# Kernel tuning notes

Hardware: AMD Instinct MI355X
Metric: run time of the kernel (lower is better)

Reference implementation:

```python
import jax, jax.numpy as jnp
import numpy as np

B, N, E, NREG, DIN, F = 16, 20000, 640000, 2000, 128, 32
NEG_SLOPE = 0.2  # PyG GATConv default negative_slope


def setup_inputs() -> dict:
    key = jax.random.key(0)
    ks = jax.random.split(key, 10)
    x = jax.random.normal(ks[0], (B, N, DIN), dtype=jnp.float32)
    edge_src = jnp.sort(jax.random.randint(ks[1], (E,), 0, NREG, dtype=jnp.int64))
    edge_dst = jax.random.randint(ks[2], (E,), 0, N, dtype=jnp.int64)
    edge_attr = jax.random.uniform(ks[3], (B, E, 1), dtype=jnp.float32)
    # GATConv parameters (heads=1, concat=False, edge_dim=1)
    W = jax.random.normal(ks[4], (DIN, F), dtype=jnp.float32) * 0.05   # lin (shared src/dst)
    att_src = jax.random.normal(ks[5], (F,), dtype=jnp.float32) * 0.1
    att_dst = jax.random.normal(ks[6], (F,), dtype=jnp.float32) * 0.1
    lin_edge = jax.random.normal(ks[7], (1, F), dtype=jnp.float32) * 0.1
    att_edge = jax.random.normal(ks[8], (F,), dtype=jnp.float32) * 0.1
    bias = jax.random.normal(ks[9], (F,), dtype=jnp.float32) * 0.01
    return {"x": x, "edge_attr": edge_attr, "W": W, "att_src": att_src,
            "att_dst": att_dst, "lin_edge": lin_edge, "att_edge": att_edge,
            "bias": bias, "edge_src": edge_src, "edge_dst": edge_dst}


def _gat_regulon(x, eattr, W, att_src, att_dst, lin_edge, att_edge, bias,
                 src, dst):
    # x: [N, DIN], eattr: [E, 1]; src/dst: [E] int (src < NREG, sorted)
    h = x @ W                                  # [N, F]
    a_src = h @ att_src                        # [N]
    a_dst = h @ att_dst                        # [N]
    # add_self_loops=True with fill_value='mean' for edge_attr
    loop_attr = jnp.broadcast_to(jnp.mean(eattr, axis=0, keepdims=True), (N, 1))
    eattr_full = jnp.concatenate([eattr, loop_attr], axis=0)         # [E+N, 1]
    sl = jnp.arange(N, dtype=src.dtype)
    src_f = jnp.concatenate([src, sl])                               # [E+N]
    dst_f = jnp.concatenate([dst, sl])                               # [E+N]
    a_edge = (eattr_full @ lin_edge) @ att_edge                      # [E+N]
    alpha = jax.nn.leaky_relu(a_src[src_f] + a_dst[dst_f] + a_edge, NEG_SLOPE)
    # segment softmax over destination nodes (self-loops => no empty segment)
    m = jax.ops.segment_max(alpha, dst_f, num_segments=N)
    ex = jnp.exp(alpha - m[dst_f])
    s = jax.ops.segment_sum(ex, dst_f, num_segments=N)
    coef = ex / s[dst_f]                                             # [E+N]
    rep = jax.ops.segment_sum(coef[:, None] * h[src_f], dst_f, num_segments=N)
    rep = rep + bias                                                 # [N, F]
    # fused regulon pooling: out[i] = rep[i] + sum_{(i->t) in E} rep[t]
    pooled = jax.ops.segment_sum(rep[dst], src, num_segments=NREG)   # [NREG, F]
    return rep[:NREG] + pooled


def reference(x, edge_attr, W, att_src, att_dst, lin_edge, att_edge, bias,
              edge_src, edge_dst):
    fn = jax.vmap(lambda xi, ei: _gat_regulon(xi, ei, W, att_src, att_dst,
                                              lin_edge, att_edge, bias,
                                              edge_src, edge_dst))
    return fn(x, edge_attr)                                          # [B, NREG, F]
```

## Files before the change

kernel.cpp:

```cpp
#include <hip/hip_runtime.h>
#include <math.h>

#define B    16
#define N    20000
#define E    640000
#define NREG 2000
#define DIN  128
#define F    32
#define NEG  0.2f
#define BF   (B * F)
#define NCHUNK 8
#define CS   2500
#define HIST_BLOCKS 1024
#define SCAT_BLOCKS 1024

typedef unsigned int uint;

__device__ inline uint bf16pair(float a, float b) {
    uint ua = __float_as_uint(a); ua = (ua + 0x7fffu + ((ua >> 16) & 1u)) >> 16;
    uint ub = __float_as_uint(b); ub = (ub + 0x7fffu + ((ub >> 16) & 1u)) >> 16;
    return ua | (ub << 16);
}
__device__ inline float bf16lo(uint v) { return __uint_as_float(v << 16); }
__device__ inline float bf16hi(uint v) { return __uint_as_float(v & 0xffff0000u); }

__global__ __launch_bounds__(256) void k_prep1(const int* __restrict__ esrc,
                                               const int* __restrict__ edst,
                                               const float* __restrict__ eattr,
                                               const float* __restrict__ lin_edge,
                                               const float* __restrict__ att_edge,
                                               int* __restrict__ counts,
                                               int* __restrict__ roff,
                                               float* __restrict__ meanb,
                                               float* __restrict__ cedge) {
    int blk = blockIdx.x;
    int t = threadIdx.x;
    if (blk < HIST_BLOCKS) {
        {
            int b = blk >> 6, sl = blk & 63;
            const float4* base = (const float4*)(eattr + (size_t)b * E + sl * 10000);
            float s = 0.f;
            for (int i = t; i < 2500; i += 256) {
                float4 v = base[i];
                s += (v.x + v.y) + (v.z + v.w);
            }
            __shared__ float sh[256];
            sh[t] = s;
            __syncthreads();
            for (int d = 128; d > 0; d >>= 1) {
                if (t < d) sh[t] += sh[t + d];
                __syncthreads();
            }
            if (t == 0) atomicAdd(&meanb[b], sh[0]);
        }
        for (int e = blk * 256 + t; e < E; e += HIST_BLOCKS * 256)
            atomicAdd(&counts[edst[e]], 1);
    } else if (blk < HIST_BLOCKS + 8) {
        int r = (blk - HIST_BLOCKS) * 256 + t;
        if (r > NREG) return;
        int lo = 0, hi = E;
        while (lo < hi) {
            int mid = (lo + hi) >> 1;
            if (esrc[mid] < r) lo = mid + 1; else hi = mid;
        }
        roff[r] = lo;
    } else {
        if (t == 0) {
            float s = 0.f;
            for (int f = 0; f < F; ++f) s += lin_edge[f] * att_edge[f];
            *cedge = s;
        }
    }
}

__global__ __launch_bounds__(1024) void k_scan(const int* __restrict__ in,
                                               int* __restrict__ out, int n) {
    __shared__ int sh[1024];
    int t = threadIdx.x;
    int chunk = (n + 1023) / 1024;
    int lo = t * chunk;
    int hi = lo + chunk; if (hi > n) hi = n;
    int local = 0;
    for (int i = lo; i < hi; ++i) local += in[i];
    sh[t] = local;
    __syncthreads();
    for (int d = 1; d < 1024; d <<= 1) {
        int v = (t >= d) ? sh[t - d] : 0;
        __syncthreads();
        sh[t] += v;
        __syncthreads();
    }
    int run = (t == 0) ? 0 : sh[t - 1];
    for (int i = lo; i < hi; ++i) { out[i] = run; run += in[i]; }
    if (t == 1023) out[n] = sh[1023];
}

__global__ __launch_bounds__(256) void k_prep2(const int* __restrict__ esrc,
                                               const int* __restrict__ edst,
                                               const int* __restrict__ off,
                                               int* __restrict__ cursor,
                                               int* __restrict__ csr_src,
                                               int* __restrict__ csr_eid,
                                               const int* __restrict__ roff,
                                               int* __restrict__ boff,
                                               int* __restrict__ pe_dst) {
    __shared__ int cnt[NCHUNK], pref[NCHUNK], cur[NCHUNK];
    int blk = blockIdx.x;
    int t = threadIdx.x;
    if (blk < SCAT_BLOCKS) {
        int e = blk * 256 + t;
        for (; e < E; e += SCAT_BLOCKS * 256) {
            int d = edst[e];
            int pos = off[d] + atomicAdd(&cursor[d], 1);
            csr_src[pos] = esrc[e];
            csr_eid[pos] = e;
        }
    } else {
        int r = blk - SCAT_BLOCKS;
        int lo = roff[r], hi = roff[r + 1];
        if (t < NCHUNK) { cnt[t] = 0; cur[t] = 0; }
        __syncthreads();
        for (int e = lo + t; e < hi; e += 256)
            atomicAdd(&cnt[edst[e] / CS], 1);
        __syncthreads();
        if (t == 0) {
            int run = 0;
            #pragma unroll
            for (int c = 0; c < NCHUNK; ++c) { pref[c] = run; run += cnt[c]; }
        }
        __syncthreads();
        if (t < NCHUNK) boff[r * NCHUNK + t] = lo + pref[t];
        if (r == 0 && t == 0) boff[NREG * NCHUNK] = E;
        for (int e = lo + t; e < hi; e += 256) {
            int d = edst[e];
            int c = d / CS;
            int pos = lo + pref[c] + atomicAdd(&cur[c], 1);
            pe_dst[pos] = d;
        }
    }
}

__global__ __launch_bounds__(256) void k_trans(const float* __restrict__ eattr,
                                               const float* __restrict__ cedge,
                                               float* __restrict__ ew) {
    __shared__ float tile[256][17];
    int e0 = blockIdx.x * 256;
    int t = threadIdx.x;
    #pragma unroll
    for (int b = 0; b < B; ++b)
        tile[t][b] = eattr[(size_t)b * E + e0 + t];
    __syncthreads();
    float c = *cedge;
    #pragma unroll
    for (int p = 0; p < 4; ++p) {
        int i4 = (p * 256 + t) * 4;
        int el = i4 >> 4, b0 = i4 & 15;
        float4 o;
        o.x = c * tile[el][b0 + 0];
        o.y = c * tile[el][b0 + 1];
        o.z = c * tile[el][b0 + 2];
        o.w = c * tile[el][b0 + 3];
        *(float4*)&ew[(size_t)e0 * 16 + i4] = o;
    }
}

#define XS_LD 260
__global__ __launch_bounds__(256) void k_gemm(const float* __restrict__ x,
                                              const float* __restrict__ W,
                                              const float* __restrict__ att_src,
                                              const float* __restrict__ att_dst,
                                              uint* __restrict__ hu,
                                              float* __restrict__ a_src,
                                              float* __restrict__ a_dst) {
    __shared__ float Ws[DIN * F];
    __shared__ float xs[32 * XS_LD];
    int t = threadIdx.x;
    int row0 = blockIdx.x * 256;
    #pragma unroll
    for (int j = 0; j < 4; ++j) {
        int idx = (t + 256 * j) * 4;
        *(float4*)&Ws[idx] = *(const float4*)&W[idx];
    }
    const int lr = t & 63;
    const int fg = t >> 6;
    float acc[4][8];
    #pragma unroll
    for (int i = 0; i < 4; ++i)
        #pragma unroll
        for (int j = 0; j < 8; ++j) acc[i][j] = 0.f;

    for (int kc = 0; kc < 4; ++kc) {
        __syncthreads();
        #pragma unroll
        for (int j = 0; j < 8; ++j) {
            int p = t + 256 * j;
            int row = p >> 3;
            int kk  = (p & 7) * 4;
            float4 g = *(const float4*)&x[(size_t)(row0 + row) * DIN + kc * 32 + kk];
            xs[(kk + 0) * XS_LD + row] = g.x;
            xs[(kk + 1) * XS_LD + row] = g.y;
            xs[(kk + 2) * XS_LD + row] = g.z;
            xs[(kk + 3) * XS_LD + row] = g.w;
        }
        __syncthreads();
        #pragma unroll
        for (int k = 0; k < 32; ++k) {
            float4 xv = *(float4*)&xs[k * XS_LD + 4 * lr];
            float4 w0 = *(float4*)&Ws[(kc * 32 + k) * F + fg * 8];
            float4 w1 = *(float4*)&Ws[(kc * 32 + k) * F + fg * 8 + 4];
            float xr[4] = {xv.x, xv.y, xv.z, xv.w};
            float wr[8] = {w0.x, w0.y, w0.z, w0.w, w1.x, w1.y, w1.z, w1.w};
            #pragma unroll
            for (int i = 0; i < 4; ++i)
                #pragma unroll
                for (int j = 0; j < 8; ++j)
                    acc[i][j] = fmaf(xr[i], wr[j], acc[i][j]);
        }
    }
    #pragma unroll
    for (int i = 0; i < 4; ++i) {
        int row = row0 + lr * 4 + i;
        int b = row / N;
        int n = row - b * N;
        uint4 o;
        o.x = bf16pair(acc[i][0], acc[i][1]);
        o.y = bf16pair(acc[i][2], acc[i][3]);
        o.z = bf16pair(acc[i][4], acc[i][5]);
        o.w = bf16pair(acc[i][6], acc[i][7]);
        *(uint4*)&hu[(size_t)n * 256 + b * 16 + fg * 4] = o;
    }
    float* red = xs;
    __syncthreads();
    #pragma unroll
    for (int i = 0; i < 4; ++i) {
        float s1 = 0.f, s2 = 0.f;
        #pragma unroll
        for (int j = 0; j < 8; ++j) {
            float as = att_src[fg * 8 + j];
            float ad = att_dst[fg * 8 + j];
            s1 = fmaf(acc[i][j], as, s1);
            s2 = fmaf(acc[i][j], ad, s2);
        }
        red[fg * 256 + lr * 4 + i]        = s1;
        red[1024 + fg * 256 + lr * 4 + i] = s2;
    }
    __syncthreads();
    {
        float s1 = red[t] + red[256 + t] + red[512 + t] + red[768 + t];
        float s2 = red[1024 + t] + red[1280 + t] + red[1536 + t] + red[1792 + t];
        int row = row0 + t;
        int b = row / N;
        int n = row - b * N;
        a_src[(size_t)n * B + b] = s1;
        a_dst[(size_t)n * B + b] = s2;
    }
}

__global__ __launch_bounds__(256) void k_rep(
    const uint* __restrict__ hu, const float* __restrict__ a_src,
    const float* __restrict__ a_dst, const float* __restrict__ ew,
    const int* __restrict__ csr_eid,
    const float* __restrict__ bias, const float* __restrict__ meanb,
    const float* __restrict__ cedge, const int* __restrict__ dst_off,
    const int* __restrict__ csr_src, uint* __restrict__ repu) {
    int i = blockIdx.x;
    int t = threadIdx.x;
    int b  = t >> 4;
    int fp = t & 15;
    float c = *cedge;
    float adst = a_dst[(size_t)i * B + b];
    float meanv = meanb[b] * (1.f / (float)E);
    float al = a_src[(size_t)i * B + b] + adst + meanv * c;
    al = al > 0.f ? al : NEG * al;
    float wself = __expf(al);
    uint hv = hu[(size_t)i * 256 + t];
    float acc0 = wself * bf16lo(hv);
    float acc1 = wself * bf16hi(hv);
    float ssum = 0.f;
    int lo = dst_off[i], hi = dst_off[i + 1];
    for (int j = lo; j < hi; j += 16) {
        int jj = j + fp;
        int idx = jj < hi ? jj : hi - 1;
        int   sv_l = csr_src[idx];
        int   ev_l = csr_eid[idx];
        float a2 = a_src[(size_t)sv_l * B + b] + adst
                 + ew[(size_t)ev_l * B + b];
        a2 = a2 > 0.f ? a2 : NEG * a2;
        float w_l = (jj < hi) ? __expf(a2) : 0.f;
        ssum += w_l;
        #pragma unroll
        for (int q = 0; q < 16; ++q) {
            float wq = __shfl(w_l, q, 16);
            int   sq = __shfl(sv_l, q, 16);
            uint v = hu[(size_t)sq * 256 + t];
            acc0 = fmaf(wq, bf16lo(v), acc0);
            acc1 = fmaf(wq, bf16hi(v), acc1);
        }
    }
    #pragma unroll
    for (int d = 1; d < 16; d <<= 1) ssum += __shfl_xor(ssum, d, 16);
    float inv = 1.f / (wself + ssum);
    repu[(size_t)i * 256 + t] = bf16pair(acc0 * inv + bias[2 * fp],
                                         acc1 * inv + bias[2 * fp + 1]);
}

__global__ __launch_bounds__(256) void k_pool(const uint* __restrict__ repu,
                                              const int* __restrict__ boff,
                                              const int* __restrict__ pe_dst,
                                              float* __restrict__ partial) {
    int key = blockIdx.x;
    int c = key / NREG;
    int r = key - c * NREG;
    int idx = r * NCHUNK + c;
    int t = threadIdx.x;
    int lo = boff[idx], hi = boff[idx + 1];
    float acc0 = 0.f, acc1 = 0.f;
    int e = lo;
    for (; e + 8 <= hi; e += 8) {
        int d0 = pe_dst[e+0], d1 = pe_dst[e+1], d2 = pe_dst[e+2], d3 = pe_dst[e+3];
        int d4 = pe_dst[e+4], d5 = pe_dst[e+5], d6 = pe_dst[e+6], d7 = pe_dst[e+7];
        uint v0 = repu[(size_t)d0 * 256 + t];
        uint v1 = repu[(size_t)d1 * 256 + t];
        uint v2 = repu[(size_t)d2 * 256 + t];
        uint v3 = repu[(size_t)d3 * 256 + t];
        uint v4 = repu[(size_t)d4 * 256 + t];
        uint v5 = repu[(size_t)d5 * 256 + t];
        uint v6 = repu[(size_t)d6 * 256 + t];
        uint v7 = repu[(size_t)d7 * 256 + t];
        acc0 += (bf16lo(v0) + bf16lo(v1)) + (bf16lo(v2) + bf16lo(v3))
              + (bf16lo(v4) + bf16lo(v5)) + (bf16lo(v6) + bf16lo(v7));
        acc1 += (bf16hi(v0) + bf16hi(v1)) + (bf16hi(v2) + bf16hi(v3))
              + (bf16hi(v4) + bf16hi(v5)) + (bf16hi(v6) + bf16hi(v7));
    }
    for (; e < hi; ++e) {
        int d = pe_dst[e];
        uint v = repu[(size_t)d * 256 + t];
        acc0 += bf16lo(v);
        acc1 += bf16hi(v);
    }
    float2 o = {acc0, acc1};
    *(float2*)&partial[((size_t)r * NCHUNK + c) * BF + 2 * t] = o;
}

__global__ __launch_bounds__(256) void k_combine(const uint* __restrict__ repu,
                                                 const float* __restrict__ partial,
                                                 float* __restrict__ out) {
    int r = blockIdx.x;
    int t = threadIdx.x;
    int b  = t >> 4;
    int fp = t & 15;
    uint v = repu[(size_t)r * 256 + t];
    float s0 = bf16lo(v), s1 = bf16hi(v);
    #pragma unroll
    for (int c = 0; c < NCHUNK; ++c) {
        float2 p = *(const float2*)&partial[((size_t)r * NCHUNK + c) * BF + 2 * t];
        s0 += p.x; s1 += p.y;
    }
    float2 o = {s0, s1};
    *(float2*)&out[(size_t)b * NREG * F + r * F + 2 * fp] = o;
}

extern "C" void kernel_launch(void* const* d_in, const int* in_sizes, int n_in,
                              void* d_out, int out_size, void* d_ws, size_t ws_size,
                              hipStream_t stream) {
    const float* x        = (const float*)d_in[0];
    const float* eattr    = (const float*)d_in[1];
    const float* W        = (const float*)d_in[2];
    const float* att_src  = (const float*)d_in[3];
    const float* att_dst  = (const float*)d_in[4];
    const float* lin_edge = (const float*)d_in[5];
    const float* att_edge = (const float*)d_in[6];
    const float* bias     = (const float*)d_in[7];
    const int*   esrc     = (const int*)d_in[8];
    const int*   edst     = (const int*)d_in[9];
    float* out = (float*)d_out;

    char* ws = (char*)d_ws;
    size_t off = 0;
    auto alloc = [&](size_t bytes) -> void* {
        void* p = ws + off;
        off = (off + bytes + 255) & ~(size_t)255;
        return p;
    };
    uint*  hu    = (uint*)alloc((size_t)N * 256 * 4);
    uint*  repu  = (uint*)alloc((size_t)N * 256 * 4);
    float* ew    = (float*)alloc((size_t)E * B * 4);
    float* a_src = (float*)alloc((size_t)N * B * 4);
    float* a_dst = (float*)alloc((size_t)N * B * 4);
    int* dst_off = (int*)alloc((size_t)(N + 1) * 4);
    int* roff    = (int*)alloc((size_t)(NREG + 1) * 4);
    int* csr_src = (int*)alloc((size_t)E * 4);
    int* csr_eid = (int*)alloc((size_t)E * 4);
    int* pe_dst  = (int*)alloc((size_t)E * 4);
    int* boff    = (int*)alloc((size_t)(NREG * NCHUNK + 1) * 4);
    char* zbase   = ws + off;
    int* counts   = (int*)alloc((size_t)N * 4);
    int* cursor   = (int*)alloc((size_t)N * 4);
    float* meanb  = (float*)alloc((size_t)B * 4);
    float* cedge  = (float*)alloc(4);
    size_t zbytes = (size_t)((ws + off) - zbase);
    float* partial = ew;

    hipMemsetAsync(zbase, 0, zbytes, stream);

    k_prep1<<<HIST_BLOCKS + 8 + 1, 256, 0, stream>>>(esrc, edst, eattr, lin_edge,
                                                     att_edge, counts, roff,
                                                     meanb, cedge);
    k_scan<<<1, 1024, 0, stream>>>(counts, dst_off, N);
    k_prep2<<<SCAT_BLOCKS + NREG, 256, 0, stream>>>(esrc, edst, dst_off, cursor,
                                                    csr_src, csr_eid,
                                                    roff, boff, pe_dst);
    k_trans<<<E / 256, 256, 0, stream>>>(eattr, cedge, ew);
    k_gemm<<<(B * N) / 256, 256, 0, stream>>>(x, W, att_src, att_dst,
                                              hu, a_src, a_dst);
    k_rep<<<N, 256, 0, stream>>>(hu, a_src, a_dst, ew, csr_eid, bias, meanb,
                                 cedge, dst_off, csr_src, repu);
    k_pool<<<NREG * NCHUNK, 256, 0, stream>>>(repu, boff, pe_dst, partial);
    k_combine<<<NREG, 256, 0, stream>>>(repu, partial, out);
}
```

Measured before the change: 547.0 us.

## Pack CSR src/eid into int2 and widen k_rep gathers to uint2 with edge split

Merges the separate csr_src and csr_eid arrays into one int2 array so each edge needs one load. k_rep is reorganised so each thread gathers 8 bytes (4 bf16 features) per source row and handles half the edges, exchanging weights through double-buffered shared memory instead of shuffles. The two edge halves are combined with a cross-half shuffle. This aims to halve gather instruction count and improve memory coalescing in the dominant aggregation kernel, at the cost of a __syncthreads per 16-edge tile. k_trans is also moved after k_gemm in the launch order.

```diff
diff --git a/kernel.cpp b/kernel.cpp
--- a/kernel.cpp
+++ b/kernel.cpp
@@ -99,8 +99,7 @@
                                                const int* __restrict__ edst,
                                                const int* __restrict__ off,
                                                int* __restrict__ cursor,
-                                               int* __restrict__ csr_src,
-                                               int* __restrict__ csr_eid,
+                                               int2* __restrict__ csr_se,
                                                const int* __restrict__ roff,
                                                int* __restrict__ boff,
                                                int* __restrict__ pe_dst) {
@@ -112,8 +111,7 @@
         for (; e < E; e += SCAT_BLOCKS * 256) {
             int d = edst[e];
             int pos = off[d] + atomicAdd(&cursor[d], 1);
-            csr_src[pos] = esrc[e];
-            csr_eid[pos] = e;
+            csr_se[pos] = make_int2(esrc[e], e);
         }
     } else {
         int r = blk - SCAT_BLOCKS;
@@ -259,49 +257,78 @@
 __global__ __launch_bounds__(256) void k_rep(
     const uint* __restrict__ hu, const float* __restrict__ a_src,
     const float* __restrict__ a_dst, const float* __restrict__ ew,
-    const int* __restrict__ csr_eid,
+    const int2* __restrict__ csr_se,
     const float* __restrict__ bias, const float* __restrict__ meanb,
     const float* __restrict__ cedge, const int* __restrict__ dst_off,
-    const int* __restrict__ csr_src, uint* __restrict__ repu) {
+    uint* __restrict__ repu) {
+    __shared__ uint2 wsh[2][4][64];
     int i = blockIdx.x;
     int t = threadIdx.x;
-    int b  = t >> 4;
-    int fp = t & 15;
+    int w = t >> 6;
+    int l = t & 63;
+    int fpA = l & 15;
+    int bA  = (w << 2) + (l >> 4);
+    int epar = l >> 5;
+    int b4   = (l >> 3) & 3;
+    int bB   = (w << 2) + b4;
+    int u    = l & 7;
+    int laneoff = bB * 8 + u;
+
     float c = *cedge;
-    float adst = a_dst[(size_t)i * B + b];
-    float meanv = meanb[b] * (1.f / (float)E);
-    float al = a_src[(size_t)i * B + b] + adst + meanv * c;
+    int lo = dst_off[i], hi = dst_off[i + 1];
+    float adstA = a_dst[i * B + bA];
+    float ssum = 0.f;
+    float acc0 = 0.f, acc1 = 0.f, acc2 = 0.f, acc3 = 0.f;
+    const uint2* hu2 = (const uint2*)hu;
+
+    int nt = 0;
+    for (int j = lo; j < hi; j += 16, ++nt) {
+        int p = nt & 1;
+        int jj = j + fpA;
+        int idx = jj < hi ? jj : hi - 1;
+        int2 se = csr_se[idx];
+        float a2 = a_src[se.x * B + bA] + adstA + ew[se.y * B + bA];
+        a2 = a2 > 0.f ? a2 : NEG * a2;
+        float wv = (jj < hi) ? __expf(a2) : 0.f;
+        ssum += wv;
+        wsh[p][w][fpA * 4 + (l >> 4)] = make_uint2(__float_as_uint(wv), (uint)se.x);
+        __syncthreads();
+        #pragma unroll
+        for (int k = 0; k < 8; ++k) {
+            uint2 ws = wsh[p][w][(2 * k + epar) * 4 + b4];
+            float wq = __uint_as_float(ws.x);
+            uint2 v = hu2[(int)ws.y * 128 + laneoff];
+            acc0 = fmaf(wq, bf16lo(v.x), acc0);
+            acc1 = fmaf(wq, bf16hi(v.x), acc1);
+            acc2 = fmaf(wq, bf16lo(v.y), acc2);
+            acc3 = fmaf(wq, bf16hi(v.y), acc3);
+        }
+    }
+    #pragma unroll
+    for (int d = 1; d < 16; d <<= 1) ssum += __shfl_xor(ssum, d, 16);
+    float Sb = __shfl(ssum, b4 << 4, 64);
+    float meanv = meanb[bB] * (1.f / (float)E);
+    float al = a_src[i * B + bB] + a_dst[i * B + bB] + meanv * c;
     al = al > 0.f ? al : NEG * al;
     float wself = __expf(al);
-    uint hv = hu[(size_t)i * 256 + t];
-    float acc0 = wself * bf16lo(hv);
-    float acc1 = wself * bf16hi(hv);
-    float ssum = 0.f;
-    int lo = dst_off[i], hi = dst_off[i + 1];
-    for (int j = lo; j < hi; j += 16) {
-        int jj = j + fp;
-        int idx = jj < hi ? jj : hi - 1;
-        int   sv_l = csr_src[idx];
-        int   ev_l = csr_eid[idx];
-        float a2 = a_src[(size_t)sv_l * B + b] + adst
-                 + ew[(size_t)ev_l * B + b];
-        a2 = a2 > 0.f ? a2 : NEG * a2;
-        float w_l = (jj < hi) ? __expf(a2) : 0.f;
-        ssum += w_l;
-        #pragma unroll
-        for (int q = 0; q < 16; ++q) {
-            float wq = __shfl(w_l, q, 16);
-            int   sq = __shfl(sv_l, q, 16);
-            uint v = hu[(size_t)sq * 256 + t];
-            acc0 = fmaf(wq, bf16lo(v), acc0);
-            acc1 = fmaf(wq, bf16hi(v), acc1);
-        }
-    }
-    #pragma unroll
-    for (int d = 1; d < 16; d <<= 1) ssum += __shfl_xor(ssum, d, 16);
-    float inv = 1.f / (wself + ssum);
-    repu[(size_t)i * 256 + t] = bf16pair(acc0 * inv + bias[2 * fp],
-                                         acc1 * inv + bias[2 * fp + 1]);
+    if (epar == 0) {
+        uint2 hv = hu2[i * 128 + laneoff];
+        acc0 = fmaf(wself, bf16lo(hv.x), acc0);
+        acc1 = fmaf(wself, bf16hi(hv.x), acc1);
+        acc2 = fmaf(wself, bf16lo(hv.y), acc2);
+        acc3 = fmaf(wself, bf16hi(hv.y), acc3);
+    }
+    acc0 += __shfl_xor(acc0, 32, 64);
+    acc1 += __shfl_xor(acc1, 32, 64);
+    acc2 += __shfl_xor(acc2, 32, 64);
+    acc3 += __shfl_xor(acc3, 32, 64);
+    if (epar == 0) {
+        float inv = 1.f / (wself + Sb);
+        uint2 o;
+        o.x = bf16pair(acc0 * inv + bias[4 * u + 0], acc1 * inv + bias[4 * u + 1]);
+        o.y = bf16pair(acc2 * inv + bias[4 * u + 2], acc3 * inv + bias[4 * u + 3]);
+        ((uint2*)repu)[i * 128 + laneoff] = o;
+    }
 }
 
 __global__ __launch_bounds__(256) void k_pool(const uint* __restrict__ repu,
@@ -389,8 +416,7 @@
     float* a_dst = (float*)alloc((size_t)N * B * 4);
     int* dst_off = (int*)alloc((size_t)(N + 1) * 4);
     int* roff    = (int*)alloc((size_t)(NREG + 1) * 4);
-    int* csr_src = (int*)alloc((size_t)E * 4);
-    int* csr_eid = (int*)alloc((size_t)E * 4);
+    int2* csr_se = (int2*)alloc((size_t)E * 8);
     int* pe_dst  = (int*)alloc((size_t)E * 4);
     int* boff    = (int*)alloc((size_t)(NREG * NCHUNK + 1) * 4);
     char* zbase   = ws + off;
@@ -408,13 +434,12 @@
                                                      meanb, cedge);
     k_scan<<<1, 1024, 0, stream>>>(counts, dst_off, N);
     k_prep2<<<SCAT_BLOCKS + NREG, 256, 0, stream>>>(esrc, edst, dst_off, cursor,
-                                                    csr_src, csr_eid,
-                                                    roff, boff, pe_dst);
-    k_trans<<<E / 256, 256, 0, stream>>>(eattr, cedge, ew);
+                                                    csr_se, roff, boff, pe_dst);
     k_gemm<<<(B * N) / 256, 256, 0, stream>>>(x, W, att_src, att_dst,
                                               hu, a_src, a_dst);
-    k_rep<<<N, 256, 0, stream>>>(hu, a_src, a_dst, ew, csr_eid, bias, meanb,
-                                 cedge, dst_off, csr_src, repu);
+    k_trans<<<E / 256, 256, 0, stream>>>(eattr, cedge, ew);
+    k_rep<<<N, 256, 0, stream>>>(hu, a_src, a_dst, ew, csr_se, bias, meanb,
+                                 cedge, dst_off, repu);
     k_pool<<<NREG * NCHUNK, 256, 0, stream>>>(repu, boff, pe_dst, partial);
     k_combine<<<NREG, 256, 0, stream>>>(repu, partial, out);
 }
```

After: 546.6 us. Within noise of the previous version (-0.1%).

## Use fp16 storage and packed half2 FMA in attention aggregation kernel

Applied to the files above, without the earlier changes.

Switches h, rep and the per-edge attention term storage from bf16/fp32 to fp16, and restructures k_rep so each thread handles 8 features with packed half2 FMAs. Each wavefront processes 4 edges at a time, using DPP and readlane broadcasts, and the four wavefronts' partials are reduced through shared memory. CSR src and edge id are packed into int2, and partial gets its own buffer. This cuts memory traffic for the gathers and edge weights, and the FMA instruction count, at the cost of fp16 range and accumulation precision for weighted sums.

```diff
diff --git a/kernel.cpp b/kernel.cpp
--- a/kernel.cpp
+++ b/kernel.cpp
@@ -1,4 +1,5 @@
 #include <hip/hip_runtime.h>
+#include <hip/hip_fp16.h>
 #include <math.h>
 
 #define B    16
@@ -16,13 +17,13 @@
 
 typedef unsigned int uint;
 
-__device__ inline uint bf16pair(float a, float b) {
-    uint ua = __float_as_uint(a); ua = (ua + 0x7fffu + ((ua >> 16) & 1u)) >> 16;
-    uint ub = __float_as_uint(b); ub = (ub + 0x7fffu + ((ub >> 16) & 1u)) >> 16;
-    return ua | (ub << 16);
-}
-__device__ inline float bf16lo(uint v) { return __uint_as_float(v << 16); }
-__device__ inline float bf16hi(uint v) { return __uint_as_float(v & 0xffff0000u); }
+__device__ inline uint f16pair(float a, float b) {
+    __half2 h = __floats2half2_rn(a, b);
+    return *(uint*)&h;
+}
+__device__ inline float2 h2f2(uint v) {
+    return __half22float2(*(__half2*)&v);
+}
 
 __global__ __launch_bounds__(256) void k_prep1(const int* __restrict__ esrc,
                                                const int* __restrict__ edst,
@@ -99,8 +100,7 @@
                                                const int* __restrict__ edst,
                                                const int* __restrict__ off,
                                                int* __restrict__ cursor,
-                                               int* __restrict__ csr_src,
-                                               int* __restrict__ csr_eid,
+                                               int2* __restrict__ csr_se,
                                                const int* __restrict__ roff,
                                                int* __restrict__ boff,
                                                int* __restrict__ pe_dst) {
@@ -112,8 +112,7 @@
         for (; e < E; e += SCAT_BLOCKS * 256) {
             int d = edst[e];
             int pos = off[d] + atomicAdd(&cursor[d], 1);
-            csr_src[pos] = esrc[e];
-            csr_eid[pos] = e;
+            csr_se[pos] = make_int2(esrc[e], e);
         }
     } else {
         int r = blk - SCAT_BLOCKS;
@@ -142,7 +141,7 @@
 
 __global__ __launch_bounds__(256) void k_trans(const float* __restrict__ eattr,
                                                const float* __restrict__ cedge,
-                                               float* __restrict__ ew) {
+                                               __half* __restrict__ ew) {
     __shared__ float tile[256][17];
     int e0 = blockIdx.x * 256;
     int t = threadIdx.x;
@@ -155,12 +154,10 @@
     for (int p = 0; p < 4; ++p) {
         int i4 = (p * 256 + t) * 4;
         int el = i4 >> 4, b0 = i4 & 15;
-        float4 o;
-        o.x = c * tile[el][b0 + 0];
-        o.y = c * tile[el][b0 + 1];
-        o.z = c * tile[el][b0 + 2];
-        o.w = c * tile[el][b0 + 3];
-        *(float4*)&ew[(size_t)e0 * 16 + i4] = o;
+        uint2 o;
+        o.x = f16pair(c * tile[el][b0 + 0], c * tile[el][b0 + 1]);
+        o.y = f16pair(c * tile[el][b0 + 2], c * tile[el][b0 + 3]);
+        *(uint2*)&ew[(size_t)e0 * 16 + i4] = o;
     }
 }
 
@@ -223,10 +220,10 @@
         int b = row / N;
         int n = row - b * N;
         uint4 o;
-        o.x = bf16pair(acc[i][0], acc[i][1]);
-        o.y = bf16pair(acc[i][2], acc[i][3]);
-        o.z = bf16pair(acc[i][4], acc[i][5]);
-        o.w = bf16pair(acc[i][6], acc[i][7]);
+        o.x = f16pair(acc[i][0], acc[i][1]);
+        o.y = f16pair(acc[i][2], acc[i][3]);
+        o.z = f16pair(acc[i][4], acc[i][5]);
+        o.w = f16pair(acc[i][6], acc[i][7]);
         *(uint4*)&hu[(size_t)n * 256 + b * 16 + fg * 4] = o;
     }
     float* red = xs;
@@ -257,51 +254,98 @@
 }
 
 __global__ __launch_bounds__(256) void k_rep(
-    const uint* __restrict__ hu, const float* __restrict__ a_src,
-    const float* __restrict__ a_dst, const float* __restrict__ ew,
-    const int* __restrict__ csr_eid,
-    const float* __restrict__ bias, const float* __restrict__ meanb,
-    const float* __restrict__ cedge, const int* __restrict__ dst_off,
-    const int* __restrict__ csr_src, uint* __restrict__ repu) {
+    const uint4* __restrict__ hu4, const float* __restrict__ a_src,
+    const float* __restrict__ a_dst, const __half* __restrict__ ew,
+    const int2* __restrict__ csr_se, const float* __restrict__ bias,
+    const float* __restrict__ meanb, const float* __restrict__ cedge,
+    const int* __restrict__ dst_off, uint4* __restrict__ repu4) {
+    __shared__ uint4 lacc[4][64];
+    __shared__ float lsum[4][64];
     int i = blockIdx.x;
     int t = threadIdx.x;
-    int b  = t >> 4;
-    int fp = t & 15;
-    float c = *cedge;
+    int wid = t >> 6;
+    int l = t & 63;
+    int b = l >> 2;
+    int q = l & 3;
     float adst = a_dst[(size_t)i * B + b];
-    float meanv = meanb[b] * (1.f / (float)E);
-    float al = a_src[(size_t)i * B + b] + adst + meanv * c;
-    al = al > 0.f ? al : NEG * al;
-    float wself = __expf(al);
-    uint hv = hu[(size_t)i * 256 + t];
-    float acc0 = wself * bf16lo(hv);
-    float acc1 = wself * bf16hi(hv);
+    int lo = dst_off[i], hi = dst_off[i + 1];
     float ssum = 0.f;
-    int lo = dst_off[i], hi = dst_off[i + 1];
-    for (int j = lo; j < hi; j += 16) {
-        int jj = j + fp;
+    __half2 zero2 = __half2half2(__float2half(0.f));
+    __half2 acc0 = zero2, acc1 = zero2, acc2 = zero2, acc3 = zero2;
+
+    for (int g0 = lo + wid * 4; g0 < hi; g0 += 16) {
+        int jj = g0 + q;
         int idx = jj < hi ? jj : hi - 1;
-        int   sv_l = csr_src[idx];
-        int   ev_l = csr_eid[idx];
-        float a2 = a_src[(size_t)sv_l * B + b] + adst
-                 + ew[(size_t)ev_l * B + b];
+        int2 se = csr_se[idx];
+        float a2 = a_src[(size_t)se.x * B + b] + adst
+                 + __half2float(ew[(size_t)se.y * B + b]);
         a2 = a2 > 0.f ? a2 : NEG * a2;
-        float w_l = (jj < hi) ? __expf(a2) : 0.f;
-        ssum += w_l;
+        float wv = (jj < hi) ? __expf(a2) : 0.f;
+        ssum += wv;
+        __half2 w2 = __half2half2(__float2half(wv));
+        uint w2u = *(uint*)&w2;
+#define REP_STEP(EIDX, CTRL) { \
+        int wei = __builtin_amdgcn_mov_dpp((int)w2u, CTRL, 0xf, 0xf, true); \
+        __half2 weh = *(__half2*)&wei; \
+        int sre = __builtin_amdgcn_readlane(se.x, EIDX); \
+        uint4 hv = hu4[(size_t)sre * 64 + l]; \
+        acc0 = __hfma2(weh, *(__half2*)&hv.x, acc0); \
+        acc1 = __hfma2(weh, *(__half2*)&hv.y, acc1); \
+        acc2 = __hfma2(weh, *(__half2*)&hv.z, acc2); \
+        acc3 = __hfma2(weh, *(__half2*)&hv.w, acc3); }
+        REP_STEP(0, 0)
+        REP_STEP(1, 85)
+        REP_STEP(2, 170)
+        REP_STEP(3, 255)
+#undef REP_STEP
+    }
+    ssum += __shfl_xor(ssum, 1, 64);
+    ssum += __shfl_xor(ssum, 2, 64);
+    if (wid) {
+        uint4 a;
+        a.x = *(uint*)&acc0; a.y = *(uint*)&acc1;
+        a.z = *(uint*)&acc2; a.w = *(uint*)&acc3;
+        lacc[wid][l] = a;
+        lsum[wid][l] = ssum;
+    }
+    __syncthreads();
+    if (wid == 0) {
+        float2 p0 = __half22float2(acc0);
+        float2 p1 = __half22float2(acc1);
+        float2 p2 = __half22float2(acc2);
+        float2 p3 = __half22float2(acc3);
         #pragma unroll
-        for (int q = 0; q < 16; ++q) {
-            float wq = __shfl(w_l, q, 16);
-            int   sq = __shfl(sv_l, q, 16);
-            uint v = hu[(size_t)sq * 256 + t];
-            acc0 = fmaf(wq, bf16lo(v), acc0);
-            acc1 = fmaf(wq, bf16hi(v), acc1);
-        }
-    }
-    #pragma unroll
-    for (int d = 1; d < 16; d <<= 1) ssum += __shfl_xor(ssum, d, 16);
-    float inv = 1.f / (wself + ssum);
-    repu[(size_t)i * 256 + t] = bf16pair(acc0 * inv + bias[2 * fp],
-                                         acc1 * inv + bias[2 * fp + 1]);
+        for (int ww = 1; ww < 4; ++ww) {
+            uint4 a = lacc[ww][l];
+            float2 u;
+            u = h2f2(a.x); p0.x += u.x; p0.y += u.y;
+            u = h2f2(a.y); p1.x += u.x; p1.y += u.y;
+            u = h2f2(a.z); p2.x += u.x; p2.y += u.y;
+            u = h2f2(a.w); p3.x += u.x; p3.y += u.y;
+            ssum += lsum[ww][l];
+        }
+        float c = *cedge;
+        float meanv = meanb[b] * (1.f / (float)E);
+        float al = a_src[(size_t)i * B + b] + adst + meanv * c;
+        al = al > 0.f ? al : NEG * al;
+        float ws = __expf(al);
+        uint4 hv = hu4[(size_t)i * 64 + l];
+        float2 u;
+        u = h2f2(hv.x); p0.x = fmaf(ws, u.x, p0.x); p0.y = fmaf(ws, u.y, p0.y);
+        u = h2f2(hv.y); p1.x = fmaf(ws, u.x, p1.x); p1.y = fmaf(ws, u.y, p1.y);
+        u = h2f2(hv.z); p2.x = fmaf(ws, u.x, p2.x); p2.y = fmaf(ws, u.y, p2.y);
+        u = h2f2(hv.w); p3.x = fmaf(ws, u.x, p3.x); p3.y = fmaf(ws, u.y, p3.y);
+        float inv = 1.f / (ssum + ws);
+        const float4* bias4 = (const float4*)bias;
+        float4 ba = bias4[q * 2];
+        float4 bb = bias4[q * 2 + 1];
+        uint4 o;
+        o.x = f16pair(fmaf(p0.x, inv, ba.x), fmaf(p0.y, inv, ba.y));
+        o.y = f16pair(fmaf(p1.x, inv, ba.z), fmaf(p1.y, inv, ba.w));
+        o.z = f16pair(fmaf(p2.x, inv, bb.x), fmaf(p2.y, inv, bb.y));
+        o.w = f16pair(fmaf(p3.x, inv, bb.z), fmaf(p3.y, inv, bb.w));
+        repu4[(size_t)i * 64 + l] = o;
+    }
 }
 
 __global__ __launch_bounds__(256) void k_pool(const uint* __restrict__ repu,
@@ -327,16 +371,16 @@
         uint v5 = repu[(size_t)d5 * 256 + t];
         uint v6 = repu[(size_t)d6 * 256 + t];
         uint v7 = repu[(size_t)d7 * 256 + t];
-        acc0 += (bf16lo(v0) + bf16lo(v1)) + (bf16lo(v2) + bf16lo(v3))
-              + (bf16lo(v4) + bf16lo(v5)) + (bf16lo(v6) + bf16lo(v7));
-        acc1 += (bf16hi(v0) + bf16hi(v1)) + (bf16hi(v2) + bf16hi(v3))
-              + (bf16hi(v4) + bf16hi(v5)) + (bf16hi(v6) + bf16hi(v7));
+        float2 u0 = h2f2(v0), u1 = h2f2(v1), u2 = h2f2(v2), u3 = h2f2(v3);
+        float2 u4 = h2f2(v4), u5 = h2f2(v5), u6 = h2f2(v6), u7 = h2f2(v7);
+        acc0 += (u0.x + u1.x) + (u2.x + u3.x) + (u4.x + u5.x) + (u6.x + u7.x);
+        acc1 += (u0.y + u1.y) + (u2.y + u3.y) + (u4.y + u5.y) + (u6.y + u7.y);
     }
     for (; e < hi; ++e) {
         int d = pe_dst[e];
-        uint v = repu[(size_t)d * 256 + t];
-        acc0 += bf16lo(v);
-        acc1 += bf16hi(v);
+        float2 u = h2f2(repu[(size_t)d * 256 + t]);
+        acc0 += u.x;
+        acc1 += u.y;
     }
     float2 o = {acc0, acc1};
     *(float2*)&partial[((size_t)r * NCHUNK + c) * BF + 2 * t] = o;
@@ -349,8 +393,8 @@
     int t = threadIdx.x;
     int b  = t >> 4;
     int fp = t & 15;
-    uint v = repu[(size_t)r * 256 + t];
-    float s0 = bf16lo(v), s1 = bf16hi(v);
+    float2 u = h2f2(repu[(size_t)r * 256 + t]);
+    float s0 = u.x, s1 = u.y;
     #pragma unroll
     for (int c = 0; c < NCHUNK; ++c) {
         float2 p = *(const float2*)&partial[((size_t)r * NCHUNK + c) * BF + 2 * t];
@@ -384,13 +428,13 @@
     };
     uint*  hu    = (uint*)alloc((size_t)N * 256 * 4);
     uint*  repu  = (uint*)alloc((size_t)N * 256 * 4);
-    float* ew    = (float*)alloc((size_t)E * B * 4);
+    __half* ew   = (__half*)alloc((size_t)E * B * 2);
+    float* partial = (float*)alloc((size_t)NREG * NCHUNK * BF * 4);
     float* a_src = (float*)alloc((size_t)N * B * 4);
     float* a_dst = (float*)alloc((size_t)N * B * 4);
     int* dst_off = (int*)alloc((size_t)(N + 1) * 4);
     int* roff    = (int*)alloc((size_t)(NREG + 1) * 4);
-    int* csr_src = (int*)alloc((size_t)E * 4);
-    int* csr_eid = (int*)alloc((size_t)E * 4);
+    int2* csr_se = (int2*)alloc((size_t)E * 8);
     int* pe_dst  = (int*)alloc((size_t)E * 4);
     int* boff    = (int*)alloc((size_t)(NREG * NCHUNK + 1) * 4);
     char* zbase   = ws + off;
@@ -399,7 +443,6 @@
     float* meanb  = (float*)alloc((size_t)B * 4);
     float* cedge  = (float*)alloc(4);
     size_t zbytes = (size_t)((ws + off) - zbase);
-    float* partial = ew;
 
     hipMemsetAsync(zbase, 0, zbytes, stream);
 
@@ -408,13 +451,12 @@
                                                      meanb, cedge);
     k_scan<<<1, 1024, 0, stream>>>(counts, dst_off, N);
     k_prep2<<<SCAT_BLOCKS + NREG, 256, 0, stream>>>(esrc, edst, dst_off, cursor,
-                                                    csr_src, csr_eid,
-                                                    roff, boff, pe_dst);
-    k_trans<<<E / 256, 256, 0, stream>>>(eattr, cedge, ew);
+                                                    csr_se, roff, boff, pe_dst);
     k_gemm<<<(B * N) / 256, 256, 0, stream>>>(x, W, att_src, att_dst,
                                               hu, a_src, a_dst);
-    k_rep<<<N, 256, 0, stream>>>(hu, a_src, a_dst, ew, csr_eid, bias, meanb,
-                                 cedge, dst_off, csr_src, repu);
+    k_trans<<<E / 256, 256, 0, stream>>>(eattr, cedge, ew);
+    k_rep<<<N, 256, 0, stream>>>((const uint4*)hu, a_src, a_dst, ew, csr_se,
+                                 bias, meanb, cedge, dst_off, (uint4*)repu);
     k_pool<<<NREG * NCHUNK, 256, 0, stream>>>(repu, boff, pe_dst, partial);
     k_combine<<<NREG, 256, 0, stream>>>(repu, partial, out);
 }
```

Result: faster. 489.0 us (-10.6%).
